# Kernel tuning notes

Measured on AMD Instinct MI355X. Metric: run time of the kernel, lower is better.

Reference implementation:

```python
import jax, jax.numpy as jnp
import numpy as np

N = 20000          # nodes
E = 640000         # edges (avg in-degree 32)
H = 8              # attention heads
CK = 32            # key/query channels per degree
CV = 32            # value channels per degree
DK = 16            # per-head key dim = (32*1 + 32*3)/8
KEY_FEATS = 128    # key_fiber.num_features = 32*1 + 32*3
DV = 4             # fused value degree dim = 1 + 3


def setup_inputs() -> dict:
    key = jax.random.key(0)
    k1, k2, k3, k4, k5 = jax.random.split(key, 5)
    return {
        "key": jax.random.normal(k1, (E, H, DK), dtype=jnp.float32),
        "query_0": jax.random.normal(k2, (N, CK, 1), dtype=jnp.float32),
        "query_1": jax.random.normal(k3, (N, CK, 3), dtype=jnp.float32),
        "value": jax.random.normal(k4, (E, CV, DV), dtype=jnp.float32),
        "edge_dst": jnp.sort(jax.random.randint(k5, (E,), 0, N, dtype=jnp.int32)),
    }


def reference(key, query_0, query_1, value, edge_dst):
    # fuse query degrees and split into heads: (N, C, 1+3) -> (N, H, DK)
    q = jnp.concatenate([query_0, query_1], axis=-1).reshape(N, H, DK)
    # e_dot_v: per-edge dot product with destination-node query -> (E, H)
    ew = jnp.einsum('ehd,ehd->eh', key, q[edge_dst]) / np.float32(np.sqrt(KEY_FEATS))
    # edge_softmax grouped by destination node (numerically stable)
    m = jax.ops.segment_max(ew, edge_dst, num_segments=N, indices_are_sorted=True)
    ex = jnp.exp(ew - m[edge_dst])
    den = jax.ops.segment_sum(ex, edge_dst, num_segments=N, indices_are_sorted=True)
    w = ex / den[edge_dst]                       # (E, H)
    # weighted sum of multi-degree values, scattered to destination nodes
    v = value.reshape(E, H, CV // H, DV)         # (E, H, C/H, DV)
    weighted = (w[:, :, None, None] * v).reshape(E, H * (CV // H) * DV)
    feat = jax.ops.segment_sum(weighted, edge_dst, num_segments=N,
                               indices_are_sorted=True).reshape(N, CV, DV)
    # unfuse_features: split last dim by degree dims (1, 3)
    return feat[..., :1], feat[..., 1:]
```

## Files before the change

### kernel.cpp

```cpp
#include <hip/hip_runtime.h>
#include <math.h>

#define NN 20000
#define EE 640000
#define TILE 32
#define NWAVES (EE / TILE)
#define STEPS (TILE / 2)

#define OUT_F4 (NN * 32)
#define L_F4   (NN * 2)
#define Z_TOT  (OUT_F4 + L_F4)

__global__ __launch_bounds__(256)
void zero_accum(float4* __restrict__ out4, float4* __restrict__ l4) {
    int i = blockIdx.x * 256 + threadIdx.x;
    float4 z = make_float4(0.f, 0.f, 0.f, 0.f);
    if (i < OUT_F4) out4[i] = z;
    else if (i < Z_TOT) l4[i - OUT_F4] = z;
}

template<int CTRL>
__device__ __forceinline__ float dpp_add(float x) {
    int y = __builtin_amdgcn_mov_dpp(__float_as_int(x), CTRL, 0xF, 0xF, false);
    return x + __int_as_float(y);
}

__global__ __launch_bounds__(256)
void attn_edges(const float* __restrict__ key,
                const float* __restrict__ q0,
                const float* __restrict__ q1,
                const float* __restrict__ val,
                const int*   __restrict__ dst,
                float*       __restrict__ out,
                float*       __restrict__ lsum)
{
    const int wid  = blockIdx.x * 4 + (threadIdx.x >> 6);
    const int lane = threadIdx.x & 63;
    const int s    = lane >> 5;
    const int cl   = lane & 31;
    const int t    = wid * TILE;

    const int dreg = dst[t + cl];

    const int prev2 = __shfl(dreg, lane - 2);
    const unsigned long long bal = __ballot(dreg != prev2);
    const unsigned mask2  = (unsigned)bal & 0xFFFFFFFCu;
    const unsigned mybits = mask2 >> s;

    const float* kp = key + (size_t)(t + s) * 128 + cl * 4;
    const float* vp = val + (size_t)(t + s) * 128 + cl * 4;
    const float scale = 0.08838834764831845f;

    int cur_n = __shfl(dreg, s * 33);
    float4 qv;
    qv.x = q0[cur_n * 32 + cl];
    qv.y = q1[cur_n * 96 + cl * 3 + 0];
    qv.z = q1[cur_n * 96 + cl * 3 + 1];
    qv.w = q1[cur_n * 96 + cl * 3 + 2];

    float  lrun = 0.f;
    float4 acc  = make_float4(0.f, 0.f, 0.f, 0.f);

    float4 kb0 = *(const float4*)(kp);        float4 vb0 = *(const float4*)(vp);
    float4 kb1 = *(const float4*)(kp + 256);  float4 vb1 = *(const float4*)(vp + 256);
    float4 kb2 = *(const float4*)(kp + 512);  float4 vb2 = *(const float4*)(vp + 512);
    float4 kb3 = *(const float4*)(kp + 768);  float4 vb3 = *(const float4*)(vp + 768);

#define STEP(J, KB, VB)                                                        \
    {                                                                          \
        const float4 kc = KB;                                                  \
        const float4 vc = VB;                                                  \
        if ((J) + 4 < STEPS) {                                                 \
            KB = *(const float4*)(kp + ((J) + 4) * 256);                       \
            VB = *(const float4*)(vp + ((J) + 4) * 256);                       \
        }                                                                      \
        if ((J) > 0 && (mybits & (1u << (2 * (J))))) {                         \
                     \
            atomicAdd(&out[cur_n * 32 + cl], acc.x);                           \
            float* o1 = out + NN * 32 + cur_n * 96 + cl * 3;                   \
            atomicAdd(o1 + 0, acc.y);                                          \
            atomicAdd(o1 + 1, acc.z);                                          \
            atomicAdd(o1 + 2, acc.w);                                          \
            if ((cl & 3) == 0) atomicAdd(&lsum[cur_n * 8 + (cl >> 2)], lrun);  \
            acc  = make_float4(0.f, 0.f, 0.f, 0.f);                            \
            lrun = 0.f;                                                        \
            cur_n = __shfl(dreg, (s << 5) + 2 * (J) + s);    \
            qv.x = q0[cur_n * 32 + cl];                                        \
            qv.y = q1[cur_n * 96 + cl * 3 + 0];                                \
            qv.z = q1[cur_n * 96 + cl * 3 + 1];                                \
            qv.w = q1[cur_n * 96 + cl * 3 + 2];                                \
        }                                                                      \
        float p = fmaf(kc.x, qv.x, fmaf(kc.y, qv.y, fmaf(kc.z, qv.z, kc.w * qv.w))); \
        p = dpp_add<0xB1>(p);                                                  \
        p = dpp_add<0x4E>(p);                                                  \
        const float w = __expf(p * scale);                                     \
        lrun += w;                                                             \
        acc.x = fmaf(w, vc.x, acc.x);                                          \
        acc.y = fmaf(w, vc.y, acc.y);                                          \
        acc.z = fmaf(w, vc.z, acc.z);                                          \
        acc.w = fmaf(w, vc.w, acc.w);                                          \
    }

    STEP(0,  kb0, vb0)
    STEP(1,  kb1, vb1)
    STEP(2,  kb2, vb2)
    STEP(3,  kb3, vb3)
    STEP(4,  kb0, vb0)
    STEP(5,  kb1, vb1)
    STEP(6,  kb2, vb2)
    STEP(7,  kb3, vb3)
    STEP(8,  kb0, vb0)
    STEP(9,  kb1, vb1)
    STEP(10, kb2, vb2)
    STEP(11, kb3, vb3)
    STEP(12, kb0, vb0)
    STEP(13, kb1, vb1)
    STEP(14, kb2, vb2)
    STEP(15, kb3, vb3)
#undef STEP

    atomicAdd(&out[cur_n * 32 + cl], acc.x);
    float* o1 = out + NN * 32 + cur_n * 96 + cl * 3;
    atomicAdd(o1 + 0, acc.y);
    atomicAdd(o1 + 1, acc.z);
    atomicAdd(o1 + 2, acc.w);
    if ((cl & 3) == 0) atomicAdd(&lsum[cur_n * 8 + (cl >> 2)], lrun);
}

__global__ __launch_bounds__(256)
void finalize(float* __restrict__ out, const float* __restrict__ lsum) {
    const int i = blockIdx.x * 256 + threadIdx.x;
    const int n = i >> 5;
    const int c = i & 31;
    const float li = lsum[n * 8 + (c >> 2)];
    const float inv = (li > 0.f) ? 1.0f / li : 0.0f;
    out[i] *= inv;
    float* o1 = out + NN * 32 + (size_t)n * 96 + c * 3;
    o1[0] *= inv;
    o1[1] *= inv;
    o1[2] *= inv;
}

extern "C" void kernel_launch(void* const* d_in, const int* in_sizes, int n_in,
                              void* d_out, int out_size, void* d_ws, size_t ws_size,
                              hipStream_t stream) {
    const float* key = (const float*)d_in[0];
    const float* q0  = (const float*)d_in[1];
    const float* q1  = (const float*)d_in[2];
    const float* val = (const float*)d_in[3];
    const int*   dst = (const int*)d_in[4];
    float* out  = (float*)d_out;
    float* lsum = (float*)d_ws;

    zero_accum<<<(Z_TOT + 255) / 256, 256, 0, stream>>>((float4*)out, (float4*)lsum);
    attn_edges<<<NWAVES / 4, 256, 0, stream>>>(key, q0, q1, val, dst, out, lsum);
    finalize<<<(NN * 32) / 256, 256, 0, stream>>>(out, lsum);
}
```

Before: 664.9 us.

## Split fused edge kernel into separate score and value passes

Splits the single edge kernel into two. The first kernel computes the per-edge, per-head exp scores and writes them to a workspace buffer. The second streams the values together with the stored weights and does the segmented atomic accumulation. Both kernels also gain a minimum-occupancy launch-bounds hint. The intent is to lower register pressure and raise occupancy in each kernel, at the cost of an extra launch, an extra pass over dst, and an E×8 weight write and read through memory.

```diff
diff --git a/kernel.cpp b/kernel.cpp
--- a/kernel.cpp
+++ b/kernel.cpp
@@ -10,6 +10,8 @@
 #define OUT_F4 (NN * 32)
 #define L_F4   (NN * 2)
 #define Z_TOT  (OUT_F4 + L_F4)
+
+#define W_OFF (NN * 8)
 
 __global__ __launch_bounds__(256)
 void zero_accum(float4* __restrict__ out4, float4* __restrict__ l4) {
@@ -25,11 +27,67 @@
     return x + __int_as_float(y);
 }
 
-__global__ __launch_bounds__(256)
-void attn_edges(const float* __restrict__ key,
+__global__ __launch_bounds__(256, 4)
+void score_pass(const float* __restrict__ key,
                 const float* __restrict__ q0,
                 const float* __restrict__ q1,
-                const float* __restrict__ val,
+                const int*   __restrict__ dst,
+                float*       __restrict__ w)
+{
+    const int wid  = blockIdx.x * 4 + (threadIdx.x >> 6);
+    const int lane = threadIdx.x & 63;
+    const int s    = lane >> 5;
+    const int cl   = lane & 31;
+    const int t    = wid * TILE;
+
+    const int dreg = dst[t + cl];
+    const int prev2 = __shfl(dreg, lane - 2);
+    const unsigned long long bal = __ballot(dreg != prev2);
+    const unsigned mask2  = (unsigned)bal & 0xFFFFFFFCu;
+    const unsigned mybits = mask2 >> s;
+
+    const float scale = 0.08838834764831845f;
+    int cur_n = __shfl(dreg, s * 33);
+    float4 qv;
+    qv.x = q0[cur_n * 32 + cl];
+    qv.y = q1[cur_n * 96 + cl * 3 + 0];
+    qv.z = q1[cur_n * 96 + cl * 3 + 1];
+    qv.w = q1[cur_n * 96 + cl * 3 + 2];
+
+    const float* kp = key + (size_t)(t + s) * 128 + cl * 4;
+    float4 kb0 = *(const float4*)(kp);
+    float4 kb1 = *(const float4*)(kp + 256);
+    float4 kb2 = *(const float4*)(kp + 512);
+    float4 kb3 = *(const float4*)(kp + 768);
+
+#define ASTEP(J, KB)                                                           \
+    {                                                                          \
+        const float4 kc = KB;                                                  \
+        if ((J) + 4 < STEPS) KB = *(const float4*)(kp + ((J) + 4) * 256);      \
+        if ((J) > 0 && (mybits & (1u << (2 * (J))))) {                         \
+            cur_n = __shfl(dreg, (s << 5) + 2 * (J) + s);                      \
+            qv.x = q0[cur_n * 32 + cl];                                        \
+            qv.y = q1[cur_n * 96 + cl * 3 + 0];                                \
+            qv.z = q1[cur_n * 96 + cl * 3 + 1];                                \
+            qv.w = q1[cur_n * 96 + cl * 3 + 2];                                \
+        }                                                                      \
+        float p = fmaf(kc.x, qv.x, fmaf(kc.y, qv.y, fmaf(kc.z, qv.z, kc.w * qv.w))); \
+        p = dpp_add<0xB1>(p);                                                  \
+        p = dpp_add<0x4E>(p);                                                  \
+        const float wgt = __expf(p * scale);                                   \
+        if ((cl & 3) == 0) w[(size_t)(t + 2 * (J) + s) * 8 + (cl >> 2)] = wgt; \
+    }
+
+    ASTEP(0,  kb0) ASTEP(1,  kb1) ASTEP(2,  kb2) ASTEP(3,  kb3)
+    ASTEP(4,  kb0) ASTEP(5,  kb1) ASTEP(6,  kb2) ASTEP(7,  kb3)
+    ASTEP(8,  kb0) ASTEP(9,  kb1) ASTEP(10, kb2) ASTEP(11, kb3)
+    ASTEP(12, kb0) ASTEP(13, kb1) ASTEP(14, kb2) ASTEP(15, kb3)
+#undef ASTEP
+}
+
+__global__ __launch_bounds__(256, 4)
+void value_pass(const float* __restrict__ val,
+                const float* __restrict__ w,
                 const int*   __restrict__ dst,
                 float*       __restrict__ out,
                 float*       __restrict__ lsum)
@@ -41,41 +99,33 @@
     const int t    = wid * TILE;
 
     const int dreg = dst[t + cl];
-
     const int prev2 = __shfl(dreg, lane - 2);
     const unsigned long long bal = __ballot(dreg != prev2);
     const unsigned mask2  = (unsigned)bal & 0xFFFFFFFCu;
     const unsigned mybits = mask2 >> s;
 
-    const float* kp = key + (size_t)(t + s) * 128 + cl * 4;
+    int cur_n = __shfl(dreg, s * 33);
+
     const float* vp = val + (size_t)(t + s) * 128 + cl * 4;
-    const float scale = 0.08838834764831845f;
-
-    int cur_n = __shfl(dreg, s * 33);
-    float4 qv;
-    qv.x = q0[cur_n * 32 + cl];
-    qv.y = q1[cur_n * 96 + cl * 3 + 0];
-    qv.z = q1[cur_n * 96 + cl * 3 + 1];
-    qv.w = q1[cur_n * 96 + cl * 3 + 2];
+    const float* wp = w + (size_t)(t + s) * 8 + (cl >> 2);
 
     float  lrun = 0.f;
     float4 acc  = make_float4(0.f, 0.f, 0.f, 0.f);
 
-    float4 kb0 = *(const float4*)(kp);        float4 vb0 = *(const float4*)(vp);
-    float4 kb1 = *(const float4*)(kp + 256);  float4 vb1 = *(const float4*)(vp + 256);
-    float4 kb2 = *(const float4*)(kp + 512);  float4 vb2 = *(const float4*)(vp + 512);
-    float4 kb3 = *(const float4*)(kp + 768);  float4 vb3 = *(const float4*)(vp + 768);
+    float4 vb0 = *(const float4*)(vp);        float wb0 = wp[0];
+    float4 vb1 = *(const float4*)(vp + 256);  float wb1 = wp[16];
+    float4 vb2 = *(const float4*)(vp + 512);  float wb2 = wp[32];
+    float4 vb3 = *(const float4*)(vp + 768);  float wb3 = wp[48];
 
-#define STEP(J, KB, VB)                                                        \
+#define BSTEP(J, VB, WB)                                                       \
     {                                                                          \
-        const float4 kc = KB;                                                  \
         const float4 vc = VB;                                                  \
+        const float wc = WB;                                                   \
         if ((J) + 4 < STEPS) {                                                 \
-            KB = *(const float4*)(kp + ((J) + 4) * 256);                       \
             VB = *(const float4*)(vp + ((J) + 4) * 256);                       \
+            WB = wp[((J) + 4) * 16];                                           \
         }                                                                      \
         if ((J) > 0 && (mybits & (1u << (2 * (J))))) {                         \
-                     \
             atomicAdd(&out[cur_n * 32 + cl], acc.x);                           \
             float* o1 = out + NN * 32 + cur_n * 96 + cl * 3;                   \
             atomicAdd(o1 + 0, acc.y);                                          \
@@ -84,40 +134,20 @@
             if ((cl & 3) == 0) atomicAdd(&lsum[cur_n * 8 + (cl >> 2)], lrun);  \
             acc  = make_float4(0.f, 0.f, 0.f, 0.f);                            \
             lrun = 0.f;                                                        \
-            cur_n = __shfl(dreg, (s << 5) + 2 * (J) + s);    \
-            qv.x = q0[cur_n * 32 + cl];                                        \
-            qv.y = q1[cur_n * 96 + cl * 3 + 0];                                \
-            qv.z = q1[cur_n * 96 + cl * 3 + 1];                                \
-            qv.w = q1[cur_n * 96 + cl * 3 + 2];                                \
+            cur_n = __shfl(dreg, (s << 5) + 2 * (J) + s);                      \
         }                                                                      \
-        float p = fmaf(kc.x, qv.x, fmaf(kc.y, qv.y, fmaf(kc.z, qv.z, kc.w * qv.w))); \
-        p = dpp_add<0xB1>(p);                                                  \
-        p = dpp_add<0x4E>(p);                                                  \
-        const float w = __expf(p * scale);                                     \
-        lrun += w;                                                             \
-        acc.x = fmaf(w, vc.x, acc.x);                                          \
-        acc.y = fmaf(w, vc.y, acc.y);                                          \
-        acc.z = fmaf(w, vc.z, acc.z);                                          \
-        acc.w = fmaf(w, vc.w, acc.w);                                          \
+        lrun += wc;                                                            \
+        acc.x = fmaf(wc, vc.x, acc.x);                                         \
+        acc.y = fmaf(wc, vc.y, acc.y);                                         \
+        acc.z = fmaf(wc, vc.z, acc.z);                                         \
+        acc.w = fmaf(wc, vc.w, acc.w);                                         \
     }
 
-    STEP(0,  kb0, vb0)
-    STEP(1,  kb1, vb1)
-    STEP(2,  kb2, vb2)
-    STEP(3,  kb3, vb3)
-    STEP(4,  kb0, vb0)
-    STEP(5,  kb1, vb1)
-    STEP(6,  kb2, vb2)
-    STEP(7,  kb3, vb3)
-    STEP(8,  kb0, vb0)
-    STEP(9,  kb1, vb1)
-    STEP(10, kb2, vb2)
-    STEP(11, kb3, vb3)
-    STEP(12, kb0, vb0)
-    STEP(13, kb1, vb1)
-    STEP(14, kb2, vb2)
-    STEP(15, kb3, vb3)
-#undef STEP
+    BSTEP(0,  vb0, wb0) BSTEP(1,  vb1, wb1) BSTEP(2,  vb2, wb2) BSTEP(3,  vb3, wb3)
+    BSTEP(4,  vb0, wb0) BSTEP(5,  vb1, wb1) BSTEP(6,  vb2, wb2) BSTEP(7,  vb3, wb3)
+    BSTEP(8,  vb0, wb0) BSTEP(9,  vb1, wb1) BSTEP(10, vb2, wb2) BSTEP(11, vb3, wb3)
+    BSTEP(12, vb0, wb0) BSTEP(13, vb1, wb1) BSTEP(14, vb2, wb2) BSTEP(15, vb3, wb3)
+#undef BSTEP
 
     atomicAdd(&out[cur_n * 32 + cl], acc.x);
     float* o1 = out + NN * 32 + cur_n * 96 + cl * 3;
@@ -151,8 +181,10 @@
     const int*   dst = (const int*)d_in[4];
     float* out  = (float*)d_out;
     float* lsum = (float*)d_ws;
+    float* w    = (float*)d_ws + W_OFF;
 
     zero_accum<<<(Z_TOT + 255) / 256, 256, 0, stream>>>((float4*)out, (float4*)lsum);
-    attn_edges<<<NWAVES / 4, 256, 0, stream>>>(key, q0, q1, val, dst, out, lsum);
+    score_pass<<<NWAVES / 4, 256, 0, stream>>>(key, q0, q1, dst, w);
+    value_pass<<<NWAVES / 4, 256, 0, stream>>>(val, w, dst, out, lsum);
     finalize<<<(NN * 32) / 256, 256, 0, stream>>>(out, lsum);
 }
```

New measurement: 715.7 us. +7.6%, slower.
